# Performance work log

Hardware: AMD Instinct MI355X
Metric: run time of the kernel (lower is better)

## Reference

```python
import jax, jax.numpy as jnp
import numpy as np

B, S, HID = 2, 2048, 2048
H, HK, D = 16, 4, 128  # num_heads, num_kv_heads, head_dim
G = H // HK            # GQA group size


def _make_rope(B, S, D):
    pos = jnp.arange(S, dtype=jnp.float32)
    inv_freq = 1.0 / (10000.0 ** (jnp.arange(0, D, 2, dtype=jnp.float32) / D))
    freqs = pos[:, None] * inv_freq[None, :]          # [S, D/2]
    emb = jnp.concatenate([freqs, freqs], axis=-1)     # [S, D]
    cos = jnp.broadcast_to(jnp.cos(emb)[None], (B, S, D))
    sin = jnp.broadcast_to(jnp.sin(emb)[None], (B, S, D))
    return cos, sin


def setup_inputs() -> dict:
    key = jax.random.key(0)
    k0, k1, k2 = jax.random.split(key, 3)
    hidden_states = jax.random.normal(k0, (B, S, HID), dtype=jnp.float32)
    cos, sin = _make_rope(B, S, D)
    w_qkv = jax.random.normal(k1, ((H + 2 * HK) * D, HID), dtype=jnp.float32) * 0.02
    b_qkv = jnp.zeros(((H + 2 * HK) * D,), dtype=jnp.float32)
    w_o = jax.random.normal(k2, (HID, HID), dtype=jnp.float32) * 0.02
    b_o = jnp.zeros((HID,), dtype=jnp.float32)
    return {"hidden_states": hidden_states, "cos": cos, "sin": sin,
            "w_qkv": w_qkv, "b_qkv": b_qkv, "w_o": w_o, "b_o": b_o}


def _rotate_half(x):
    x1, x2 = jnp.split(x, 2, axis=-1)
    return jnp.concatenate([-x2, x1], axis=-1)


def reference(hidden_states, cos, sin, w_qkv, b_qkv, w_o, b_o):
    b, s, _ = hidden_states.shape
    qkv = jnp.einsum('bsh,oh->bso', hidden_states, w_qkv) + b_qkv
    q, k, v = jnp.split(qkv, [H * D, (H + HK) * D], axis=-1)
    # [B, heads, S, D]
    q = q.reshape(b, s, H, D).transpose(0, 2, 1, 3)
    k = k.reshape(b, s, HK, D).transpose(0, 2, 1, 3)
    v = v.reshape(b, s, HK, D).transpose(0, 2, 1, 3)
    # RoPE (cos/sin broadcast over head axis)
    c = cos[:, None, :, :]
    sn = sin[:, None, :, :]
    q = q * c + _rotate_half(q) * sn
    k = k * c + _rotate_half(k) * sn
    # GQA attention without materializing repeated K/V: group q heads
    qg = q.reshape(b, HK, G, s, D)
    scale = 1.0 / jnp.sqrt(jnp.float32(D))
    scores = jnp.einsum('bkgqd,bkpd->bkgqp', qg, k) * scale  # [B,HK,G,S,S]
    probs = jax.nn.softmax(scores, axis=-1)
    out = jnp.einsum('bkgqp,bkpd->bkgqd', probs, v)           # [B,HK,G,S,D]
    out = out.reshape(b, H, s, D).transpose(0, 2, 1, 3).reshape(b, s, H * D)
    return jnp.einsum('bsh,oh->bso', out, w_o) + b_o
```

## Files before the change

kernel.cpp:

```cpp
#include <hip/hip_runtime.h>
#include <hip/hip_bf16.h>
#include <stdint.h>

typedef __bf16 bf16x8 __attribute__((ext_vector_type(8)));
typedef float f32x4 __attribute__((ext_vector_type(4)));
typedef float f32x16 __attribute__((ext_vector_type(16)));
typedef float f32x4v __attribute__((ext_vector_type(4)));
typedef unsigned short u16;
typedef unsigned int u32;
typedef u16 u16x8 __attribute__((ext_vector_type(8)));
typedef u32 u32x4 __attribute__((ext_vector_type(4)));

#define B_ 2
#define S_ 2048
#define HID_ 2048
#define H_ 16
#define HK_ 4
#define D_ 128
#define NQKV_ 3072

__device__ __forceinline__ u16 f2bf(float f) {
  u32 u = __builtin_bit_cast(u32, f);
  u32 r = (u + 0x7fffu + ((u >> 16) & 1u)) >> 16;
  return (u16)r;
}
__device__ __forceinline__ float bf2f(u16 v) {
  u32 u = ((u32)v) << 16;
  return __builtin_bit_cast(float, u);
}
__device__ __forceinline__ u32 cvtpk(float lo, float hi) {
  u32 r;
  asm("v_cvt_pk_bf16_f32 %0, %1, %2" : "=v"(r) : "v"(lo), "v"(hi));
  return r;
}
__device__ __forceinline__ void gload_lds16(const void* g, void* l) {
  __builtin_amdgcn_global_load_lds((const __attribute__((address_space(1))) void*)g,
                                   (__attribute__((address_space(3))) void*)l, 16, 0, 0);
}

__global__ __launch_bounds__(256) void k_f32_to_bf16(const float* __restrict__ in,
                                                     u16* __restrict__ out, int n8) {
  for (int i = blockIdx.x * 256 + threadIdx.x; i < n8; i += gridDim.x * 256) {
    const f32x4v* p = (const f32x4v*)(in + (size_t)i * 8);
    f32x4v a = p[0], b = p[1];
    u16x8 w;
    w[0] = f2bf(a[0]); w[1] = f2bf(a[1]); w[2] = f2bf(a[2]); w[3] = f2bf(a[3]);
    w[4] = f2bf(b[0]); w[5] = f2bf(b[1]); w[6] = f2bf(b[2]); w[7] = f2bf(b[3]);
    *(u16x8*)(out + (size_t)i * 8) = w;
  }
}

template <int ISSUES>
__device__ __forceinline__ void stage_half(const u16* __restrict__ src, int K, char* ldsb, int tid) {
#pragma unroll
  for (int i = 0; i < ISSUES; ++i) {
    int off = i * 8192 + tid * 16;
    int r = off >> 7, cb = off & 127;
    int scb = cb ^ ((r & 7) << 4);
    gload_lds16((const char*)(src + (size_t)r * K) + scb, ldsb + i * 8192 + (tid & ~63) * 16);
  }
}

template <int BM, typename CT>
__global__ __launch_bounds__(512, 1) void k_gemm8p(const u16* __restrict__ A, const u16* __restrict__ Bm,
                                                   const float* __restrict__ bias, CT* __restrict__ C,
                                                   int M, int N, int K) {
  constexpr int HAR = BM / 2;
  constexpr int AHB = HAR * 128;
  constexpr int AISS = AHB / 8192;
  constexpr int MREP = BM / 32;
  constexpr int MQ = MREP / 4;
  constexpr int DB = 2 * AHB + 32768;
  __shared__ __attribute__((aligned(16))) char lds[2 * DB];
  const int tid = threadIdx.x, lane = tid & 63;
  const int wid = tid >> 6, wm = wid >> 2, wn = wid & 3;
  const int l15 = lane & 15, l4 = lane >> 4;
  const int row0 = blockIdx.y * BM, col0 = blockIdx.x * 256;
  const int NT = K >> 6;

  f32x4 acc[MREP][4] = {};

  auto stageA = [&](int t, int h) {
    stage_half<AISS>(A + (size_t)(row0 + h * HAR) * K + t * 64, K, lds + (t & 1) * DB + h * AHB, tid);
  };
  auto stageB = [&](int t, int h) {
    stage_half<2>(Bm + (size_t)(col0 + h * 128) * K + t * 64, K, lds + (t & 1) * DB + 2 * AHB + h * 16384, tid);
  };

  stageA(0, 0); stageA(0, 1); stageB(0, 0); stageB(0, 1);
  if (NT > 1) { stageB(1, 0); stageB(1, 1); }
  if (NT > 1) asm volatile("s_waitcnt vmcnt(4)" ::: "memory");
  else        asm volatile("s_waitcnt vmcnt(0)" ::: "memory");
  __builtin_amdgcn_s_barrier();

  const char* myA = lds + wm * AHB;
  const char* myB = lds + 2 * AHB + (wn >> 1) * 16384;
  const int rBb = (wn & 1) * 64;

  for (int t = 0; t < NT; ++t) {
    const int d = t & 1;
    const char* Ab = myA + d * DB;
    const char* Bb = myB + d * DB;
    bf16x8 bfr[4][2];
#pragma unroll
    for (int j = 0; j < 4; ++j) {
      if (j == 0) {
#pragma unroll
        for (int n = 0; n < 4; ++n)
#pragma unroll
          for (int ks = 0; ks < 2; ++ks) {
            int r = rBb + n * 16 + l15;
            bfr[n][ks] = *(const bf16x8*)(Bb + r * 128 + ((ks * 64 + l4 * 16) ^ ((r & 7) << 4)));
          }
      }
      bf16x8 afr[MQ][2];
#pragma unroll
      for (int mq = 0; mq < MQ; ++mq)
#pragma unroll
        for (int ks = 0; ks < 2; ++ks) {
          int r = (j * MQ + mq) * 16 + l15;
          afr[mq][ks] = *(const bf16x8*)(Ab + r * 128 + ((ks * 64 + l4 * 16) ^ ((r & 7) << 4)));
        }
      if (j == 0) { if (t + 1 < NT) stageA(t + 1, 0); }
      else if (j == 1) { if (t + 1 < NT) stageA(t + 1, 1); }
      else if (j == 2) { if (t + 2 < NT) stageB(t + 2, 0); }
      else {
        if (t + 2 < NT) { stageB(t + 2, 1); asm volatile("s_waitcnt vmcnt(4)" ::: "memory"); }
        else             asm volatile("s_waitcnt vmcnt(0)" ::: "memory");
      }
      __builtin_amdgcn_s_barrier();
      asm volatile("s_waitcnt lgkmcnt(0)" ::: "memory");
      __builtin_amdgcn_s_setprio(1);
#pragma unroll
      for (int mq = 0; mq < MQ; ++mq)
#pragma unroll
        for (int ks = 0; ks < 2; ++ks)
#pragma unroll
          for (int n = 0; n < 4; ++n)
            acc[j * MQ + mq][n] =
                __builtin_amdgcn_mfma_f32_16x16x32_bf16(afr[mq][ks], bfr[n][ks], acc[j * MQ + mq][n], 0, 0, 0);
      __builtin_amdgcn_s_setprio(0);
      __builtin_amdgcn_s_barrier();
    }
  }

#pragma unroll
  for (int m = 0; m < MREP; ++m) {
    int grow = row0 + wm * HAR + m * 16 + l4 * 4;
#pragma unroll
    for (int n = 0; n < 4; ++n) {
      int gcol = col0 + wn * 64 + n * 16 + l15;
      float bv = bias[gcol];
#pragma unroll
      for (int r2 = 0; r2 < 4; ++r2) {
        float v = acc[m][n][r2] + bv;
        if constexpr (sizeof(CT) == 2) C[(size_t)(grow + r2) * N + gcol] = (CT)f2bf(v);
        else                           C[(size_t)(grow + r2) * N + gcol] = v;
      }
    }
  }
}

__global__ __launch_bounds__(256) void k_rope_split(const u16* __restrict__ qkv,
                                                    const float* __restrict__ cosb,
                                                    const float* __restrict__ sinb,
                                                    u16* __restrict__ Qb, u16* __restrict__ Kb,
                                                    u16* __restrict__ Vt) {
  const int bs = blockIdx.x;
  const int b = bs >> 11, s = bs & 2047;
  const size_t base = (size_t)bs * NQKV_;
  const size_t cs = (size_t)bs * D_;
  const float qscale = 0.08838834764831845f;
  for (int p = threadIdx.x; p < H_ * 64; p += 256) {
    int h = p >> 6, d = p & 63;
    float f1 = bf2f(qkv[base + h * D_ + d]);
    float f2 = bf2f(qkv[base + h * D_ + 64 + d]);
    float c1 = cosb[cs + d], s1 = sinb[cs + d];
    float c2 = cosb[cs + 64 + d], s2 = sinb[cs + 64 + d];
    size_t o = ((size_t)(b * H_ + h) * S_ + s) * D_ + d;
    Qb[o] = f2bf((f1 * c1 - f2 * s1) * qscale);
    Qb[o + 64] = f2bf((f2 * c2 + f1 * s2) * qscale);
  }
  for (int p = threadIdx.x; p < HK_ * 64; p += 256) {
    int hk = p >> 6, d = p & 63;
    float f1 = bf2f(qkv[base + H_ * D_ + hk * D_ + d]);
    float f2 = bf2f(qkv[base + H_ * D_ + hk * D_ + 64 + d]);
    float c1 = cosb[cs + d], s1 = sinb[cs + d];
    float c2 = cosb[cs + 64 + d], s2 = sinb[cs + 64 + d];
    size_t o = ((size_t)(b * HK_ + hk) * S_ + s) * D_ + d;
    Kb[o] = f2bf(f1 * c1 - f2 * s1);
    Kb[o + 64] = f2bf(f2 * c2 + f1 * s2);
  }
  for (int p = threadIdx.x; p < HK_ * D_; p += 256) {
    int hk = p >> 7, d = p & 127;
    Vt[((size_t)(b * HK_ + hk) * D_ + d) * S_ + s] = qkv[base + H_ * D_ + HK_ * D_ + hk * D_ + d];
  }
}

__global__ __launch_bounds__(512, 2) void k_attn(const u16* __restrict__ Qb, const u16* __restrict__ Kb,
                                                 const u16* __restrict__ Vt, u16* __restrict__ Ob) {
  __shared__ __attribute__((aligned(16))) char lds[65536];
  char* lKc = lds;
  char* lVc = lds + 16384;
  const int qt = blockIdx.x;
  const int bh = blockIdx.y;
  const int b = bh >> 4, h = bh & 15, hk = h >> 2;
  const int tid = threadIdx.x, lane = tid & 63, wid = tid >> 6;
  const int l31 = lane & 31, hi = lane >> 5;

  const int qrow = qt * 256 + wid * 32 + l31;
  const u16* qptr = Qb + ((size_t)(b * H_ + h) * S_ + qrow) * D_;
  bf16x8 qf[8];
#pragma unroll
  for (int ks = 0; ks < 8; ++ks) qf[ks] = *(const bf16x8*)(qptr + ks * 16 + hi * 8);

  const u16* kbase = Kb + (size_t)(b * HK_ + hk) * S_ * D_;
  const u16* vbase = Vt + (size_t)(b * HK_ + hk) * D_ * S_;

  int krow[2], kc[2], vrow[2], vc[2];
#pragma unroll
  for (int i = 0; i < 2; ++i) {
    int s = tid + i * 512;
    krow[i] = s >> 4; kc[i] = s & 15;
    vrow[i] = s >> 3; vc[i] = s & 7;
  }

  f32x16 o[4] = {};
  float mrun = -1e30f, lrun = 0.f;

  bf16x8 kreg[2], vreg[2];
#pragma unroll
  for (int i = 0; i < 2; ++i) {
    kreg[i] = *(const bf16x8*)(kbase + (size_t)krow[i] * D_ + kc[i] * 8);
    vreg[i] = *(const bf16x8*)(vbase + (size_t)vrow[i] * S_ + vc[i] * 8);
  }
#pragma unroll
  for (int i = 0; i < 2; ++i) {
    *(bf16x8*)(lKc + ((krow[i] * 256 + kc[i] * 16) ^ ((krow[i] & 15) << 4))) = kreg[i];
    *(bf16x8*)(lVc + ((vrow[i] * 128 + vc[i] * 16) ^ ((vrow[i] & 7) << 4))) = vreg[i];
  }
  __syncthreads();

  for (int kt = 0; kt < 32; ++kt) {
    if (kt < 31) {
#pragma unroll
      for (int i = 0; i < 2; ++i) {
        kreg[i] = *(const bf16x8*)(kbase + (size_t)((kt + 1) * 64 + krow[i]) * D_ + kc[i] * 8);
        vreg[i] = *(const bf16x8*)(vbase + (size_t)vrow[i] * S_ + (kt + 1) * 64 + vc[i] * 8);
      }
    }

    f32x16 sc[2] = {};
    __builtin_amdgcn_s_setprio(1);
#pragma unroll
    for (int ks = 0; ks < 8; ++ks) {
#pragma unroll
      for (int T = 0; T < 2; ++T) {
        int row = T * 32 + l31;
        bf16x8 kf = *(const bf16x8*)(lKc + ((row * 256 + ks * 32 + hi * 16) ^ ((row & 15) << 4)));
        sc[T] = __builtin_amdgcn_mfma_f32_32x32x16_bf16(kf, qf[ks], sc[T], 0, 0, 0);
      }
    }
    __builtin_amdgcn_s_setprio(0);

    float pmax = sc[0][0];
#pragma unroll
    for (int r = 1; r < 16; ++r) pmax = fmaxf(pmax, sc[0][r]);
#pragma unroll
    for (int r = 0; r < 16; ++r) pmax = fmaxf(pmax, sc[1][r]);
    pmax = fmaxf(pmax, __shfl_xor(pmax, 32));
    if (__any(pmax > mrun + 8.f)) {
      float mn = fmaxf(mrun, pmax);
      float alpha = __expf(mrun - mn);
      mrun = mn;
      lrun *= alpha;
#pragma unroll
      for (int dt = 0; dt < 4; ++dt)
#pragma unroll
        for (int r = 0; r < 16; ++r) o[dt][r] *= alpha;
    }
    float rs = 0.f;
#pragma unroll
    for (int T = 0; T < 2; ++T)
#pragma unroll
      for (int r = 0; r < 16; ++r) {
        float p = __expf(sc[T][r] - mrun);
        sc[T][r] = p;
        rs += p;
      }
    rs += __shfl_xor(rs, 32);
    lrun += rs;

    bf16x8 pf[4];
#pragma unroll
    for (int T = 0; T < 2; ++T) {
#pragma unroll
      for (int g = 0; g < 2; ++g) {
        u32 a0 = cvtpk(sc[T][8 * g + 0], sc[T][8 * g + 1]);
        u32 a1 = cvtpk(sc[T][8 * g + 2], sc[T][8 * g + 3]);
        u32 a2 = cvtpk(sc[T][8 * g + 4], sc[T][8 * g + 5]);
        u32 a3 = cvtpk(sc[T][8 * g + 6], sc[T][8 * g + 7]);
        u32 x0 = (u32)__shfl_xor((int)a0, 32);
        u32 x1 = (u32)__shfl_xor((int)a1, 32);
        u32 x2 = (u32)__shfl_xor((int)a2, 32);
        u32 x3 = (u32)__shfl_xor((int)a3, 32);
        u32 s0 = hi ? x2 : a0;
        u32 s1 = hi ? x3 : a1;
        u32 s2 = hi ? a2 : x0;
        u32 s3 = hi ? a3 : x1;
        u32x4 w = {s0, s1, s2, s3};
        pf[T * 2 + g] = __builtin_bit_cast(bf16x8, w);
      }
    }

    __builtin_amdgcn_s_setprio(1);
#pragma unroll
    for (int ks2 = 0; ks2 < 4; ++ks2) {
#pragma unroll
      for (int dt = 0; dt < 4; ++dt) {
        int row = dt * 32 + l31;
        bf16x8 vf = *(const bf16x8*)(lVc + ((row * 128 + ks2 * 32 + hi * 16) ^ ((row & 7) << 4)));
        o[dt] = __builtin_amdgcn_mfma_f32_32x32x16_bf16(vf, pf[ks2], o[dt], 0, 0, 0);
      }
    }
    __builtin_amdgcn_s_setprio(0);

    __syncthreads();
    if (kt < 31) {
#pragma unroll
      for (int i = 0; i < 2; ++i) {
        *(bf16x8*)(lKc + ((krow[i] * 256 + kc[i] * 16) ^ ((krow[i] & 15) << 4))) = kreg[i];
        *(bf16x8*)(lVc + ((vrow[i] * 128 + vc[i] * 16) ^ ((vrow[i] & 7) << 4))) = vreg[i];
      }
    }
    __syncthreads();
  }

  float inv = 1.0f / lrun;
  char* myreg = lds + wid * 8192;
#pragma unroll
  for (int dt = 0; dt < 4; ++dt)
#pragma unroll
    for (int t = 0; t < 8; ++t) {
      u32 w = cvtpk(o[dt][2 * t] * inv, o[dt][2 * t + 1] * inv);
      int d0 = dt * 32 + 2 * (t & 1) + 8 * (t >> 1) + 4 * hi;
      *(u32*)(myreg + ((l31 * 256 + d0 * 2) ^ ((l31 & 15) << 4))) = w;
    }
  asm volatile("s_waitcnt lgkmcnt(0)");
  {
    int q = lane >> 1, hf = lane & 1;
    int srow = qt * 256 + wid * 32 + q;
    u16* orow = Ob + ((size_t)(b * S_ + srow)) * HID_ + h * 128 + hf * 64;
#pragma unroll
    for (int i = 0; i < 8; ++i) {
      bf16x8 vv = *(const bf16x8*)(myreg + ((q * 256 + hf * 128 + i * 16) ^ ((q & 15) << 4)));
      *(bf16x8*)(orow + i * 8) = vv;
    }
  }
}

extern "C" void kernel_launch(void* const* d_in, const int* in_sizes, int n_in,
                              void* d_out, int out_size, void* d_ws, size_t ws_size,
                              hipStream_t stream) {
  const float* hs = (const float*)d_in[0];
  const float* cosb = (const float*)d_in[1];
  const float* sinb = (const float*)d_in[2];
  const float* w_qkv = (const float*)d_in[3];
  const float* b_qkv = (const float*)d_in[4];
  const float* w_o = (const float*)d_in[5];
  const float* b_o = (const float*)d_in[6];
  float* out = (float*)d_out;

  char* ws = (char*)d_ws;
  u16* Xb    = (u16*)ws;
  u16* Wqkvb = (u16*)(ws + 16777216);
  u16* Wob   = (u16*)(ws + 29360128);
  u16* qkvb  = (u16*)(ws + 37748736);
  u16* Qb    = (u16*)(ws + 62914560);
  u16* Kb    = (u16*)(ws + 79691776);
  u16* Vt    = (u16*)(ws + 83886080);
  u16* Ob = Xb;

  hipLaunchKernelGGL(k_f32_to_bf16, dim3(2048), dim3(256), 0, stream, hs, Xb, (B_ * S_ * HID_) / 8);
  hipLaunchKernelGGL(k_f32_to_bf16, dim3(1536), dim3(256), 0, stream, w_qkv, Wqkvb, (NQKV_ * HID_) / 8);
  hipLaunchKernelGGL(k_f32_to_bf16, dim3(1024), dim3(256), 0, stream, w_o, Wob, (HID_ * HID_) / 8);
  hipLaunchKernelGGL((k_gemm8p<256, u16>), dim3(NQKV_ / 256, (B_ * S_) / 256), dim3(512), 0, stream,
                     Xb, Wqkvb, b_qkv, qkvb, B_ * S_, NQKV_, HID_);
  hipLaunchKernelGGL(k_rope_split, dim3(B_ * S_), dim3(256), 0, stream, qkvb, cosb, sinb, Qb, Kb, Vt);
  hipLaunchKernelGGL(k_attn, dim3(S_ / 256, B_ * H_), dim3(512), 0, stream, Qb, Kb, Vt, Ob);
  hipLaunchKernelGGL((k_gemm8p<128, float>), dim3(HID_ / 256, (B_ * S_) / 128), dim3(512), 0, stream,
                     Ob, Wob, b_o, out, B_ * S_, HID_, HID_);
}
```

Before: 222.0 us.

## Double-buffer K/V LDS tiles in attention and merge conversion kernels

```diff
diff --git a/kernel.cpp b/kernel.cpp
--- a/kernel.cpp
+++ b/kernel.cpp
@@ -38,15 +38,23 @@
                                    (__attribute__((address_space(3))) void*)l, 16, 0, 0);
 }
 
-__global__ __launch_bounds__(256) void k_f32_to_bf16(const float* __restrict__ in,
-                                                     u16* __restrict__ out, int n8) {
-  for (int i = blockIdx.x * 256 + threadIdx.x; i < n8; i += gridDim.x * 256) {
-    const f32x4v* p = (const f32x4v*)(in + (size_t)i * 8);
-    f32x4v a = p[0], b = p[1];
+__global__ __launch_bounds__(256) void k_cvt3(const float* __restrict__ a, u16* __restrict__ oa, int na,
+                                              const float* __restrict__ b, u16* __restrict__ ob, int nb,
+                                              const float* __restrict__ c, u16* __restrict__ oc, int nc) {
+  int total = na + nb + nc;
+  for (int i = blockIdx.x * 256 + threadIdx.x; i < total; i += gridDim.x * 256) {
+    const float* src;
+    u16* dst;
+    int j = i;
+    if (j < na) { src = a; dst = oa; }
+    else if (j < na + nb) { j -= na; src = b; dst = ob; }
+    else { j -= na + nb; src = c; dst = oc; }
+    const f32x4v* p = (const f32x4v*)(src + (size_t)j * 8);
+    f32x4v x = p[0], y = p[1];
     u16x8 w;
-    w[0] = f2bf(a[0]); w[1] = f2bf(a[1]); w[2] = f2bf(a[2]); w[3] = f2bf(a[3]);
-    w[4] = f2bf(b[0]); w[5] = f2bf(b[1]); w[6] = f2bf(b[2]); w[7] = f2bf(b[3]);
-    *(u16x8*)(out + (size_t)i * 8) = w;
+    w[0] = f2bf(x[0]); w[1] = f2bf(x[1]); w[2] = f2bf(x[2]); w[3] = f2bf(x[3]);
+    w[4] = f2bf(y[0]); w[5] = f2bf(y[1]); w[6] = f2bf(y[2]); w[7] = f2bf(y[3]);
+    *(u16x8*)(dst + (size_t)j * 8) = w;
   }
 }
 
@@ -200,8 +208,6 @@
 __global__ __launch_bounds__(512, 2) void k_attn(const u16* __restrict__ Qb, const u16* __restrict__ Kb,
                                                  const u16* __restrict__ Vt, u16* __restrict__ Ob) {
   __shared__ __attribute__((aligned(16))) char lds[65536];
-  char* lKc = lds;
-  char* lVc = lds + 16384;
   const int qt = blockIdx.x;
   const int bh = blockIdx.y;
   const int b = bh >> 4, h = bh & 15, hk = h >> 2;
@@ -236,12 +242,16 @@
   }
 #pragma unroll
   for (int i = 0; i < 2; ++i) {
-    *(bf16x8*)(lKc + ((krow[i] * 256 + kc[i] * 16) ^ ((krow[i] & 15) << 4))) = kreg[i];
-    *(bf16x8*)(lVc + ((vrow[i] * 128 + vc[i] * 16) ^ ((vrow[i] & 7) << 4))) = vreg[i];
+    *(bf16x8*)(lds + ((krow[i] * 256 + kc[i] * 16) ^ ((krow[i] & 15) << 4))) = kreg[i];
+    *(bf16x8*)(lds + 16384 + ((vrow[i] * 128 + vc[i] * 16) ^ ((vrow[i] & 7) << 4))) = vreg[i];
   }
   __syncthreads();
 
   for (int kt = 0; kt < 32; ++kt) {
+    const int cur = kt & 1;
+    const char* lKc = lds + cur * 32768;
+    const char* lVc = lKc + 16384;
+
     if (kt < 31) {
 #pragma unroll
       for (int i = 0; i < 2; ++i) {
@@ -325,12 +335,13 @@
     }
     __builtin_amdgcn_s_setprio(0);
 
-    __syncthreads();
     if (kt < 31) {
+      char* nK = lds + (cur ^ 1) * 32768;
+      char* nV = nK + 16384;
 #pragma unroll
       for (int i = 0; i < 2; ++i) {
-        *(bf16x8*)(lKc + ((krow[i] * 256 + kc[i] * 16) ^ ((krow[i] & 15) << 4))) = kreg[i];
-        *(bf16x8*)(lVc + ((vrow[i] * 128 + vc[i] * 16) ^ ((vrow[i] & 7) << 4))) = vreg[i];
+        *(bf16x8*)(nK + ((krow[i] * 256 + kc[i] * 16) ^ ((krow[i] & 15) << 4))) = kreg[i];
+        *(bf16x8*)(nV + ((vrow[i] * 128 + vc[i] * 16) ^ ((vrow[i] & 7) << 4))) = vreg[i];
       }
     }
     __syncthreads();
@@ -381,9 +392,10 @@
   u16* Vt    = (u16*)(ws + 83886080);
   u16* Ob = Xb;
 
-  hipLaunchKernelGGL(k_f32_to_bf16, dim3(2048), dim3(256), 0, stream, hs, Xb, (B_ * S_ * HID_) / 8);
-  hipLaunchKernelGGL(k_f32_to_bf16, dim3(1536), dim3(256), 0, stream, w_qkv, Wqkvb, (NQKV_ * HID_) / 8);
-  hipLaunchKernelGGL(k_f32_to_bf16, dim3(1024), dim3(256), 0, stream, w_o, Wob, (HID_ * HID_) / 8);
+  hipLaunchKernelGGL(k_cvt3, dim3(2048), dim3(256), 0, stream,
+                     hs, Xb, (B_ * S_ * HID_) / 8,
+                     w_qkv, Wqkvb, (NQKV_ * HID_) / 8,
+                     w_o, Wob, (HID_ * HID_) / 8);
   hipLaunchKernelGGL((k_gemm8p<256, u16>), dim3(NQKV_ / 256, (B_ * S_) / 256), dim3(512), 0, stream,
                      Xb, Wqkvb, b_qkv, qkvb, B_ * S_, NQKV_, HID_);
   hipLaunchKernelGGL(k_rope_split, dim3(B_ * S_), dim3(256), 0, stream, qkvb, cosb, sinb, Qb, Kb, Vt);
```

Result: no change. 219.7 us (-1.1%).
